# Kernel optimization log

Measured on AMD Instinct MI355X. Metric: run time of the kernel, lower is better.

The kernel has to match this reference:

```python
import jax, jax.numpy as jnp
import numpy as np
from jax import lax

K = 8
SCALE = 100.0

# ---- straight-through binarizers (match torch custom Functions) ----
@jax.custom_vjp
def bin_w(x):
    return jnp.sign(x)

def _bin_w_fwd(x):
    return jnp.sign(x), None

def _bin_w_bwd(_, g):
    return (g,)  # identity STE

bin_w.defvjp(_bin_w_fwd, _bin_w_bwd)

@jax.custom_vjp
def bin_a(x):
    return jnp.sign(x)

def _bin_a_fwd(x):
    return jnp.sign(x), x

def _bin_a_bwd(x, g):
    return (g * jnp.clip(2.0 - jnp.abs(2.0 * x), 0.0, None),)

bin_a.defvjp(_bin_a_fwd, _bin_a_bwd)

# ---- SDP sampling with custom backward (grad_z scaled by sqrt(scale)) ----
@jax.custom_vjp
def sdp(m, z, rv):
    # m: (N,), z: (K,N), rv: (1,K) -> w: (N,)
    return (rv @ z)[0] + m

def _sdp_fwd(m, z, rv):
    return (rv @ z)[0] + m, rv

def _sdp_bwd(rv, g):
    grad_m = g
    grad_z = (rv.T @ g[None, :]) * np.sqrt(SCALE)  # (K,N)
    return (grad_m, grad_z, jnp.zeros_like(rv))

sdp.defvjp(_sdp_fwd, _sdp_bwd)

def _forward(x, M, Z, alpha, rv):
    N = M.size
    m = M.reshape(N)          # (N,)
    z = Z.reshape(K, N)       # (K,N)
    # no_grad normalization of m,z data: value changes, gradient passes through identity
    A = m * m + jnp.sum(z * z, axis=0) / SCALE
    inv = lax.rsqrt(A)
    m_used = m + lax.stop_gradient(m * inv - m)
    z_used = z + lax.stop_gradient(z * inv - z)
    w = sdp(m_used, z_used, rv)               # (N,)
    bw = bin_w(w).reshape(M.shape)            # (O,I,3,3) in {-1,+1}
    ba = bin_a(x)                             # (B,C,H,W) in {-1,+1}
    out = lax.conv_general_dilated(
        ba, bw, window_strides=(1, 1), padding=((1, 1), (1, 1)),
        dimension_numbers=('NCHW', 'OIHW', 'NCHW'))
    return out * alpha  # alpha (O,1,1) broadcasts over (B,O,H,W)

def setup_inputs() -> dict:
    key = jax.random.key(0)
    k1, k2, k3, k4, k5 = jax.random.split(key, 5)
    x = jax.random.normal(k1, (64, 256, 28, 28), dtype=jnp.float32)
    M = jax.random.normal(k2, (256, 256, 3, 3), dtype=jnp.float32)
    Z = jax.random.normal(k3, (8, 256, 256, 3, 3), dtype=jnp.float32)
    alpha = jax.random.uniform(k4, (256, 1, 1), dtype=jnp.float32)
    rv = jax.random.normal(k5, (1, 8), dtype=jnp.float32) * np.float32(1.0 / np.sqrt(SCALE))
    return {"x": x, "M": M, "Z": Z, "alpha": alpha, "rv": rv}

def reference(x, M, Z, alpha, rv):
    return _forward(x, M, Z, alpha, rv)
```

## Files before the change

### kernel.cpp

```cpp
#include <hip/hip_runtime.h>
#include <stdint.h>

typedef unsigned int uint32;
typedef unsigned char u8;
typedef int v4i __attribute__((ext_vector_type(4)));

#define BB 64
#define CC 256
#define OO 256
#define HH 28
#define WW 28
#define HWP 784
#define NWT 589824
#define HP 30
#define XBSTR (HP * HP * 256)
#define WTAP (256 * 256)
#define PPIX 272

__global__ __launch_bounds__(256) void cast_x_kernel(
    const float* __restrict__ x, u8* __restrict__ xi8) {
  __shared__ u8 srow[30 * 260];
  const int hp = blockIdx.x;
  const int b  = blockIdx.y;
  const int tid = threadIdx.x;
  const int wp = tid & 31;
  const int cq0 = tid >> 5;
  const bool interior = (hp >= 1) && (hp <= 28) && (wp >= 1) && (wp <= 28);
  const float* xp =
      x + (((size_t)b * 256) * 28 + (hp - 1)) * 28 + (wp - 1);
  if (wp < HP) {
#pragma unroll
    for (int it = 0; it < 8; ++it) {
      const int cq = it * 8 + cq0;
      uint32 v = 0;
      if (interior) {
        const float* p = xp + (size_t)(cq * 4) * HWP;
        uint32 b0 = (p[0] > 0.f) ? 0x01u : 0xFFu;
        uint32 b1 = (p[HWP] > 0.f) ? 0x01u : 0xFFu;
        uint32 b2 = (p[2 * HWP] > 0.f) ? 0x01u : 0xFFu;
        uint32 b3 = (p[3 * HWP] > 0.f) ? 0x01u : 0xFFu;
        v = b0 | (b1 << 8) | (b2 << 16) | (b3 << 24);
      }
      *(uint32*)(&srow[wp * 260 + cq * 4]) = v;
    }
  }
  __syncthreads();
  u8* rowbase = xi8 + (size_t)b * XBSTR + (size_t)hp * 7680;
#pragma unroll
  for (int i = 0; i < 2; ++i) {
    int c = tid + i * 256;
    if (c < 480) {
      uint4 v = *(const uint4*)(&srow[(c >> 4) * 260 + (c & 15) * 16]);
      *(uint4*)(rowbase + (size_t)c * 16) = v;
    }
  }
}

__global__ __launch_bounds__(256) void cast_w_kernel(
    const float* __restrict__ M, const float* __restrict__ Z,
    const float* __restrict__ rv, u8* __restrict__ wi8) {
  __shared__ float sacc[2304];
  const int o = blockIdx.x;
  const int tid = threadIdx.x;
  const size_t base = (size_t)o * 2304;
  float r[8];
#pragma unroll
  for (int k = 0; k < 8; ++k) r[k] = rv[k];
#pragma unroll
  for (int ii = 0; ii < 9; ++ii) {
    int i = tid + ii * 256;
    float s = M[base + i];
#pragma unroll
    for (int k = 0; k < 8; ++k) s += r[k] * Z[(size_t)k * NWT + base + i];
    sacc[i] = s;
  }
  __syncthreads();
  const int c = tid;
#pragma unroll
  for (int t = 0; t < 9; ++t) {
    float s = sacc[c * 9 + t];
    wi8[((size_t)t * 256 + o) * 256 + c] = (s > 0.f) ? (u8)1 : (u8)0xFF;
  }
}

#define LOADG(g_, AF, BF)                                                      \
  {                                                                            \
    const int tap_ = (g_) >> 2, ks_ = (g_) & 3;                                \
    const int toff_ =                                                          \
        ((tap_ / 3) * 30 + (tap_ % 3)) * PPIX + ks_ * 64;                      \
    _Pragma("unroll") for (int ot = 0; ot < 4; ++ot)                           \
        (BF)[ot] = *(const v4i*)(Bb + ((size_t)tap_ * WTAP) +                  \
                                 (bvoff + ot * 4096 + ks_ * 64));              \
    _Pragma("unroll") for (int mt = 0; mt < 7; ++mt)                           \
        (AF)[mt] = *(const v4i*)(&albs[lb[mt] + toff_]);                       \
  }

#define MFMAG(AF, BF)                                                          \
  {                                                                            \
    _Pragma("unroll") for (int mt = 0; mt < 7; ++mt)                           \
        _Pragma("unroll") for (int ot = 0; ot < 4; ++ot)                       \
            acc[mt][ot] = __builtin_amdgcn_mfma_i32_16x16x64_i8(               \
                (AF)[mt], (BF)[ot], acc[mt][ot], 0, 0, 0);                     \
  }

#define SGB() __builtin_amdgcn_sched_barrier(0)

__global__ __launch_bounds__(256, 2) void conv_mfma_kernel(
    const u8* __restrict__ xi8, const u8* __restrict__ wi8,
    const float* __restrict__ alpha, float* __restrict__ out) {
  __shared__ u8 albs[6 * 30 * PPIX];
  const int tid = threadIdx.x;
  const int lane = tid & 63;
  const int wv = tid >> 6;
  const int l15 = lane & 15;
  const int lk  = lane >> 4;
  const int pixb = blockIdx.x * 112;
  const int h0   = blockIdx.x * 4;
  const int b    = blockIdx.y;

  {
    const u8* gsrc = xi8 + (size_t)b * XBSTR + (size_t)h0 * 7680;
#pragma unroll
    for (int i = 0; i < 12; ++i) {
      int c = tid + i * 256;
      if (c < 2880) {
        uint4 v = *(const uint4*)(gsrc + (size_t)c * 16);
        *(uint4*)(&albs[(c >> 4) * PPIX + (c & 15) * 16]) = v;
      }
    }
  }
  __syncthreads();

  int lb[7];
#pragma unroll
  for (int mt = 0; mt < 7; ++mt) {
    int p = pixb + mt * 16 + l15;
    int h = p / 28, w = p - h * 28;
    lb[mt] = ((h - h0) * 30 + w) * PPIX + lk * 16;
  }
  const u8* Bb = wi8 + wv * (64 * 256);
  const int bvoff = l15 * 256 + lk * 16;

  float aval[4];
#pragma unroll
  for (int ot = 0; ot < 4; ++ot) aval[ot] = alpha[wv * 64 + ot * 16 + l15];

  v4i acc[7][4];
#pragma unroll
  for (int mt = 0; mt < 7; ++mt)
#pragma unroll
    for (int ot = 0; ot < 4; ++ot) acc[mt][ot] = v4i{0, 0, 0, 0};

  v4i A0[7], B0[4], A1[7], B1[4];
  LOADG(0, A0, B0);
#pragma unroll
  for (int g = 0; g < 36; g += 2) {
    LOADG(g + 1, A1, B1);
    SGB();
    MFMAG(A0, B0);
    SGB();
    if (g + 2 < 36) LOADG(g + 2, A0, B0);
    SGB();
    MFMAG(A1, B1);
    SGB();
  }

#pragma unroll
  for (int mt = 0; mt < 7; ++mt) {
    const int prow = pixb + mt * 16 + lk * 4;
#pragma unroll
    for (int ot = 0; ot < 4; ++ot) {
      float* op = out +
          ((size_t)b * 256 + (wv * 64 + ot * 16 + l15)) * HWP + prow;
      float4 vst;
      vst.x = aval[ot] * (float)acc[mt][ot][0];
      vst.y = aval[ot] * (float)acc[mt][ot][1];
      vst.z = aval[ot] * (float)acc[mt][ot][2];
      vst.w = aval[ot] * (float)acc[mt][ot][3];
      *(float4*)op = vst;
    }
  }
}

extern "C" void kernel_launch(void* const* d_in, const int* in_sizes, int n_in,
                              void* d_out, int out_size, void* d_ws,
                              size_t ws_size, hipStream_t stream) {
  const float* x     = (const float*)d_in[0];
  const float* M     = (const float*)d_in[1];
  const float* Z     = (const float*)d_in[2];
  const float* alpha = (const float*)d_in[3];
  const float* rv    = (const float*)d_in[4];
  float* out = (float*)d_out;

  u8* xi8 = (u8*)d_ws;
  u8* wi8 = (u8*)d_ws + 14745600;

  cast_x_kernel<<<dim3(HP, BB), 256, 0, stream>>>(x, xi8);
  cast_w_kernel<<<dim3(256), 256, 0, stream>>>(M, Z, rv, wi8);
  conv_mfma_kernel<<<dim3(7, BB), 256, 0, stream>>>(xi8, wi8, alpha, out);
}
```

Baseline: 163.1 us.

## Fuse activation binarization into the conv kernel's shared-memory load

Drops the separate cast_x kernel and its padded int8 workspace buffer. The conv kernel now reads fp32 activations directly, applies the sign, and writes packed int8 values into its shared-memory tile, handling halo padding inline. This removes one launch plus the write and re-read of the intermediate int8 tensor. In exchange, overlapping halo rows are loaded from fp32 memory more than once, the prologue uses only part of the block's threads for many strided loads, and this load latency is not overlapped with the MFMA loop.

Measured after the change: 175.9 us. +7.9%, slower.

```diff
diff --git a/kernel.cpp b/kernel.cpp
--- a/kernel.cpp
+++ b/kernel.cpp
@@ -12,49 +12,8 @@
 #define WW 28
 #define HWP 784
 #define NWT 589824
-#define HP 30
-#define XBSTR (HP * HP * 256)
 #define WTAP (256 * 256)
 #define PPIX 272
-
-__global__ __launch_bounds__(256) void cast_x_kernel(
-    const float* __restrict__ x, u8* __restrict__ xi8) {
-  __shared__ u8 srow[30 * 260];
-  const int hp = blockIdx.x;
-  const int b  = blockIdx.y;
-  const int tid = threadIdx.x;
-  const int wp = tid & 31;
-  const int cq0 = tid >> 5;
-  const bool interior = (hp >= 1) && (hp <= 28) && (wp >= 1) && (wp <= 28);
-  const float* xp =
-      x + (((size_t)b * 256) * 28 + (hp - 1)) * 28 + (wp - 1);
-  if (wp < HP) {
-#pragma unroll
-    for (int it = 0; it < 8; ++it) {
-      const int cq = it * 8 + cq0;
-      uint32 v = 0;
-      if (interior) {
-        const float* p = xp + (size_t)(cq * 4) * HWP;
-        uint32 b0 = (p[0] > 0.f) ? 0x01u : 0xFFu;
-        uint32 b1 = (p[HWP] > 0.f) ? 0x01u : 0xFFu;
-        uint32 b2 = (p[2 * HWP] > 0.f) ? 0x01u : 0xFFu;
-        uint32 b3 = (p[3 * HWP] > 0.f) ? 0x01u : 0xFFu;
-        v = b0 | (b1 << 8) | (b2 << 16) | (b3 << 24);
-      }
-      *(uint32*)(&srow[wp * 260 + cq * 4]) = v;
-    }
-  }
-  __syncthreads();
-  u8* rowbase = xi8 + (size_t)b * XBSTR + (size_t)hp * 7680;
-#pragma unroll
-  for (int i = 0; i < 2; ++i) {
-    int c = tid + i * 256;
-    if (c < 480) {
-      uint4 v = *(const uint4*)(&srow[(c >> 4) * 260 + (c & 15) * 16]);
-      *(uint4*)(rowbase + (size_t)c * 16) = v;
-    }
-  }
-}
 
 __global__ __launch_bounds__(256) void cast_w_kernel(
     const float* __restrict__ M, const float* __restrict__ Z,
@@ -106,7 +65,7 @@
 #define SGB() __builtin_amdgcn_sched_barrier(0)
 
 __global__ __launch_bounds__(256, 2) void conv_mfma_kernel(
-    const u8* __restrict__ xi8, const u8* __restrict__ wi8,
+    const float* __restrict__ x, const u8* __restrict__ wi8,
     const float* __restrict__ alpha, float* __restrict__ out) {
   __shared__ u8 albs[6 * 30 * PPIX];
   const int tid = threadIdx.x;
@@ -119,13 +78,33 @@
   const int b    = blockIdx.y;
 
   {
-    const u8* gsrc = xi8 + (size_t)b * XBSTR + (size_t)h0 * 7680;
+    const int wp = tid & 31;
+    const int rseg = tid >> 5;
+    if (rseg < 6 && wp < 30) {
+      const int imgrow = h0 + rseg - 1;
+      const bool rowok = (imgrow >= 0) && (imgrow < HH);
+      const bool interior = rowok && (wp >= 1) && (wp <= WW);
+      const float* xp =
+          x + ((size_t)(b * CC) * HH + (rowok ? imgrow : 0)) * WW + (wp - 1);
+      u8* dst = &albs[(rseg * 30 + wp) * PPIX];
 #pragma unroll
-    for (int i = 0; i < 12; ++i) {
-      int c = tid + i * 256;
-      if (c < 2880) {
-        uint4 v = *(const uint4*)(gsrc + (size_t)c * 16);
-        *(uint4*)(&albs[(c >> 4) * PPIX + (c & 15) * 16]) = v;
+      for (int c4 = 0; c4 < 16; ++c4) {
+        uint32 vv[4];
+#pragma unroll
+        for (int q = 0; q < 4; ++q) {
+          const int cq = c4 * 4 + q;
+          uint32 v = 0;
+          if (interior) {
+            const float* p = xp + (size_t)(cq * 4) * HWP;
+            uint32 b0 = (p[0] > 0.f) ? 0x01u : 0xFFu;
+            uint32 b1 = (p[HWP] > 0.f) ? 0x01u : 0xFFu;
+            uint32 b2 = (p[2 * HWP] > 0.f) ? 0x01u : 0xFFu;
+            uint32 b3 = (p[3 * HWP] > 0.f) ? 0x01u : 0xFFu;
+            v = b0 | (b1 << 8) | (b2 << 16) | (b3 << 24);
+          }
+          vv[q] = v;
+        }
+        *(uint4*)(dst + c4 * 16) = make_uint4(vv[0], vv[1], vv[2], vv[3]);
       }
     }
   }
@@ -192,10 +171,8 @@
   const float* rv    = (const float*)d_in[4];
   float* out = (float*)d_out;
 
-  u8* xi8 = (u8*)d_ws;
-  u8* wi8 = (u8*)d_ws + 14745600;
+  u8* wi8 = (u8*)d_ws;
 
-  cast_x_kernel<<<dim3(HP, BB), 256, 0, stream>>>(x, xi8);
   cast_w_kernel<<<dim3(256), 256, 0, stream>>>(M, Z, rv, wi8);
-  conv_mfma_kernel<<<dim3(7, BB), 256, 0, stream>>>(xi8, wi8, alpha, out);
+  conv_mfma_kernel<<<dim3(7, BB), 256, 0, stream>>>(x, wi8, alpha, out);
 }
```
